# Optimization experiments

Hardware: AMD Instinct MI355X
Metric: run time of the kernel (lower is better)

Reference implementation:

```python
import jax, jax.numpy as jnp
import numpy as np

H = 1024      # embe_size / hidden size
L = 2         # layer_num
LBL = 5       # label_size
B, S = 64, 512


def setup_inputs() -> dict:
    key = jax.random.key(0)
    ks = jax.random.split(key, 7)
    sc = 1.0 / np.sqrt(H)
    inputs = jax.random.normal(ks[0], (B, S, H), dtype=jnp.float32)
    Wx = jax.random.uniform(ks[1], (L, H, 4 * H), minval=-sc, maxval=sc, dtype=jnp.float32)
    bx = jax.random.uniform(ks[2], (L, 4 * H), minval=-sc, maxval=sc, dtype=jnp.float32)
    Wh = jax.random.uniform(ks[3], (L, H, 4 * H), minval=-sc, maxval=sc, dtype=jnp.float32)
    bh = jax.random.uniform(ks[4], (L, 4 * H), minval=-sc, maxval=sc, dtype=jnp.float32)
    scp = 1.0 / np.sqrt(H)
    Wp = jax.random.uniform(ks[5], (H, LBL), minval=-scp, maxval=scp, dtype=jnp.float32)
    bp = jax.random.uniform(ks[6], (LBL,), minval=-scp, maxval=scp, dtype=jnp.float32)
    return {"inputs": inputs, "Wx": Wx, "bx": bx, "Wh": Wh, "bh": bh, "Wp": Wp, "bp": bp}


def _lstm_forward(inputs, Wx, bx, Wh, bh, Wp, bp):
    # inputs: [B,S,H] -> time-major [S,B,H]
    x = jnp.transpose(inputs, (1, 0, 2))
    n_layers = Wx.shape[0]
    bsz, hid = x.shape[1], Wx.shape[1]
    for l in range(n_layers):
        Wh_l, bh_l = Wh[l], bh[l]
        # precompute input->gate projection for all timesteps: [S,B,4H]
        xg = jnp.einsum('sbh,hg->sbg', x, Wx[l]) + bx[l]

        def step(carry, xg_t):
            h, c = carry
            feat = xg_t + h @ Wh_l + bh_l
            i, f, g, o = jnp.split(feat, 4, axis=-1)
            c = jax.nn.sigmoid(f) * c + jax.nn.sigmoid(i) * jnp.tanh(g)
            h = jnp.tanh(c) * jax.nn.sigmoid(o)
            return (h, c), h

        h0 = jnp.zeros((bsz, hid), dtype=x.dtype)
        _, x = jax.lax.scan(step, (h0, h0), xg)
        # dropout is identity at inference (eval mode)
    # max-pool over time (max_pool1d over full seq), then classify
    pooled = jnp.max(x, axis=0)  # [B,H]
    return pooled @ Wp + bp      # [B,label_size]


def reference(inputs, Wx, bx, Wh, bh, Wp, bp):
    return _lstm_forward(inputs, Wx, bx, Wh, bh, Wp, bp)
```

## Files before the change

### kernel.cpp

```cpp
#include <hip/hip_runtime.h>
#include <hip/hip_bf16.h>

typedef _Float16 half8 __attribute__((ext_vector_type(8)));
typedef _Float16 half4v __attribute__((ext_vector_type(4)));
typedef float f32x4 __attribute__((ext_vector_type(4)));
typedef unsigned int u32;
typedef unsigned long long u64;

#define BB 64
#define SS 512
#define HH 1024
#define G4 4096
#define SLOT 65536

#define SB_ARR(g) ((g) * 32)
#define SB_GLB 256
#define SB_GO(g) (288 + (g) * 32)
#define NSTEP 514

__device__ __forceinline__ float sigmf(float x) { return 1.0f / (1.0f + __expf(-x)); }
__device__ __forceinline__ float tanhfast(float x) { return 2.0f / (1.0f + __expf(-2.0f * x)) - 1.0f; }

__device__ __forceinline__ u32 aload(const u32* p) {
  return __hip_atomic_load(p, __ATOMIC_RELAXED, __HIP_MEMORY_SCOPE_AGENT);
}
__device__ __forceinline__ void wait_ge(const u32* p, u32 tgt) {
  while (aload(p) < tgt) __builtin_amdgcn_s_sleep(1);
}
__device__ __forceinline__ u32 aadd(u32* p) {
  return __hip_atomic_fetch_add(p, 1u, __ATOMIC_RELAXED, __HIP_MEMORY_SCOPE_AGENT);
}
__device__ __forceinline__ void astore(u32* p, u32 v) {
  __hip_atomic_store(p, v, __ATOMIC_RELAXED, __HIP_MEMORY_SCOPE_AGENT);
}
__device__ __forceinline__ void astore64(u64* p, u64 v) {
  __hip_atomic_store(p, v, __ATOMIC_RELAXED, __HIP_MEMORY_SCOPE_AGENT);
}

__global__ __launch_bounds__(256) void convert_x_kernel(const float* __restrict__ in,
                                                        _Float16* __restrict__ x16) {
  size_t idx = (size_t)blockIdx.x * 256 + threadIdx.x;
  int h4 = (int)(idx & 255);
  int s  = (int)((idx >> 8) & 511);
  int b  = (int)(idx >> 17);
  const float4* src = (const float4*)in;
  float4 v = src[((size_t)b * SS + s) * 256 + h4];
  half4v hv = { (_Float16)v.x, (_Float16)v.y, (_Float16)v.z, (_Float16)v.w };
  *(half4v*)(x16 + ((size_t)s * BB + b) * HH + (size_t)h4 * 4) = hv;
}

__global__ __launch_bounds__(256) void convert_w_kernel(const float* __restrict__ Wx,
                                                        const float* __restrict__ Wh,
                                                        _Float16* __restrict__ wT) {
  __shared__ float tile[32][33];
  int m = blockIdx.x >> 12;
  int t = blockIdx.x & 4095;
  int tn = t & 127, tk = t >> 7;
  int l = m & 1, which = m >> 1;
  const float* src = (which ? Wh : Wx) + (size_t)l * HH * G4;
  int tx = threadIdx.x & 31, ty = threadIdx.x >> 5;
#pragma unroll
  for (int p = 0; p < 4; ++p) {
    int k = tk * 32 + ty + 8 * p, n = tn * 32 + tx;
    tile[ty + 8 * p][tx] = src[(size_t)k * G4 + n];
  }
  __syncthreads();
  _Float16* dst = wT + (size_t)m * G4 * HH;
#pragma unroll
  for (int p = 0; p < 4; ++p) {
    int n = tn * 32 + ty + 8 * p, k = tk * 32 + tx;
    dst[(size_t)n * HH + k] = (_Float16)tile[tx][ty + 8 * p];
  }
}

__global__ __launch_bounds__(512, 2) void lstm_flow(
    const _Float16* __restrict__ x16, const _Float16* __restrict__ wT,
    const float* __restrict__ bx, const float* __restrict__ bh,
    _Float16* __restrict__ h1buf, _Float16* __restrict__ h2buf,
    float* __restrict__ hmax, u32* __restrict__ tag1, u32* __restrict__ tag2) {
  __shared__ float part[8][32][72];
  __shared__ float red[64][37];

  const int bid = blockIdx.x;
  const int layer = bid >> 7;
  const int j = bid & 127;
  const int tid = threadIdx.x;
  const int w = tid >> 6, l = tid & 63;
  const int l15 = l & 15, lg = l >> 4;
  const int rep = bid & 1;

  const _Float16* wTe = wT + (size_t)layer * G4 * HH;
  const _Float16* wTr = wT + (size_t)(2 + layer) * G4 * HH;
  const int kbase = w * 128;
  half8 Be[8], Br[8];
#pragma unroll
  for (int kk = 0; kk < 4; ++kk)
#pragma unroll
    for (int c = 0; c < 2; ++c) {
      int nl = 16 * c + l15;
      size_t gcol = (size_t)((nl & 3) * HH + 8 * j + (nl >> 2));
      Be[kk * 2 + c] = *(const half8*)(wTe + gcol * HH + kbase + 32 * kk + 8 * lg);
      Br[kk * 2 + c] = *(const half8*)(wTr + gcol * HH + kbase + 32 * kk + 8 * lg);
    }

  float bsv[32];
  float cst[8], hx[8];
#pragma unroll
  for (int cp = 0; cp < 8; ++cp) {
    cst[cp] = 0.f;
    hx[cp] = -2.f;
#pragma unroll
    for (int g = 0; g < 4; ++g)
      bsv[cp * 4 + g] = bx[layer * G4 + g * HH + 8 * j + cp] + bh[layer * G4 + g * HH + 8 * j + cp];
  }

#define POLL(TAGS, SLOTT)                                                              \
  {                                                                                    \
    const u32* tp = (TAGS) + ((size_t)(SLOTT) * 2 + rep) * 128 + 16 * w + l15;         \
    while (true) {                                                                     \
      u32 v = (l < 16) ? aload(tp) : 1u;                                               \
      if (__all(v != 0)) break;                                                        \
      __builtin_amdgcn_s_sleep(2);                                                     \
    }                                                                                  \
    asm volatile("" ::: "memory");                                                     \
  }

#pragma unroll 1
  for (int t = 0; t < SS; ++t) {
    f32x4 acc[8];
#pragma unroll
    for (int i = 0; i < 8; ++i) acc[i] = (f32x4){0.f, 0.f, 0.f, 0.f};

    {
      const _Float16* Ae;
      if (layer == 0) {
        Ae = x16 + (size_t)t * SLOT;
      } else {
        POLL(tag1, t + 1)
        Ae = h1buf + (size_t)(t + 1) * SLOT;
      }
      const _Float16* aep = Ae + (size_t)l15 * HH + kbase + 8 * lg;
      half8 a[16];
#pragma unroll
      for (int rf = 0; rf < 4; ++rf)
#pragma unroll
        for (int kk = 0; kk < 4; ++kk)
          a[rf * 4 + kk] = *(const half8*)(aep + (size_t)(16 * rf) * HH + 32 * kk);
#pragma unroll
      for (int rf = 0; rf < 4; ++rf)
#pragma unroll
        for (int kk = 0; kk < 4; ++kk) {
          acc[rf * 2 + 0] = __builtin_amdgcn_mfma_f32_16x16x32_f16(a[rf * 4 + kk], Be[kk * 2 + 0], acc[rf * 2 + 0], 0, 0, 0);
          acc[rf * 2 + 1] = __builtin_amdgcn_mfma_f32_16x16x32_f16(a[rf * 4 + kk], Be[kk * 2 + 1], acc[rf * 2 + 1], 0, 0, 0);
        }
    }

    {
      const _Float16* Ah;
      if (layer == 0) {
        if (t >= 1) POLL(tag1, t)
        Ah = h1buf + (size_t)t * SLOT;
      } else {
        if (t >= 1) POLL(tag2, t)
        Ah = h2buf + (size_t)t * SLOT;
      }
      const _Float16* ahp = Ah + (size_t)l15 * HH + kbase + 8 * lg;
      half8 a[16];
#pragma unroll
      for (int rf = 0; rf < 4; ++rf)
#pragma unroll
        for (int kk = 0; kk < 4; ++kk)
          a[rf * 4 + kk] = *(const half8*)(ahp + (size_t)(16 * rf) * HH + 32 * kk);
#pragma unroll
      for (int rf = 0; rf < 4; ++rf)
#pragma unroll
        for (int kk = 0; kk < 4; ++kk) {
          acc[rf * 2 + 0] = __builtin_amdgcn_mfma_f32_16x16x32_f16(a[rf * 4 + kk], Br[kk * 2 + 0], acc[rf * 2 + 0], 0, 0, 0);
          acc[rf * 2 + 1] = __builtin_amdgcn_mfma_f32_16x16x32_f16(a[rf * 4 + kk], Br[kk * 2 + 1], acc[rf * 2 + 1], 0, 0, 0);
        }
    }

#pragma unroll
    for (int rf = 0; rf < 4; ++rf)
#pragma unroll
      for (int c = 0; c < 2; ++c)
        *(f32x4*)&part[w][16 * c + l15][16 * rf + 4 * lg] = acc[rf * 2 + c];
    __syncthreads();

    {
      int col = tid >> 4, rq = tid & 15;
      f32x4 s = {0.f, 0.f, 0.f, 0.f};
#pragma unroll
      for (int ww = 0; ww < 8; ++ww)
        s += *(const f32x4*)&part[ww][col][4 * rq];
      red[4 * rq + 0][col] = s[0];
      red[4 * rq + 1][col] = s[1];
      red[4 * rq + 2][col] = s[2];
      red[4 * rq + 3][col] = s[3];
    }
    __syncthreads();

    if (w == 0) {
      u32 pk[4];
#pragma unroll
      for (int cp = 0; cp < 8; ++cp) {
        float vi = red[l][4 * cp + 0] + bsv[cp * 4 + 0];
        float vf = red[l][4 * cp + 1] + bsv[cp * 4 + 1];
        float vg = red[l][4 * cp + 2] + bsv[cp * 4 + 2];
        float vo = red[l][4 * cp + 3] + bsv[cp * 4 + 3];
        float ig = sigmf(vi), fg = sigmf(vf), gg = tanhfast(vg), og = sigmf(vo);
        float cn = fg * cst[cp] + ig * gg;
        cst[cp] = cn;
        float hn = tanhfast(cn) * og;
        if (layer == 1) hx[cp] = fmaxf(hx[cp], hn);
        u32 hb = (u32)__builtin_bit_cast(unsigned short, (_Float16)hn);
        if ((cp & 1) == 0) pk[cp >> 1] = hb;
        else pk[cp >> 1] |= hb << 16;
      }
      if (layer == 0 || t < SS - 1) {
        _Float16* hout = (layer == 0 ? h1buf : h2buf) + (size_t)(t + 1) * SLOT;
        u64* dst = (u64*)(hout + (size_t)l * HH + 8 * j);
        astore64(dst,     ((u64)pk[1] << 32) | pk[0]);
        astore64(dst + 1, ((u64)pk[3] << 32) | pk[2]);
        asm volatile("s_waitcnt vmcnt(0)" ::: "memory");
        if (l == 0) {
          u32* tg = (layer == 0 ? tag1 : tag2);
          astore(tg + ((size_t)(t + 1) * 2 + 0) * 128 + j, 1u);
          astore(tg + ((size_t)(t + 1) * 2 + 1) * 128 + j, 1u);
        }
      }
    }
  }
#undef POLL

  if (layer == 1 && w == 0) {
    float* hp = hmax + (size_t)l * HH + 8 * j;
    *(float4*)hp = (float4){hx[0], hx[1], hx[2], hx[3]};
    *(float4*)(hp + 4) = (float4){hx[4], hx[5], hx[6], hx[7]};
  }
}

__global__ __launch_bounds__(512, 2) void lstm_safe(
    const _Float16* __restrict__ x16, const _Float16* __restrict__ wT,
    const float* __restrict__ bx, const float* __restrict__ bh,
    _Float16* __restrict__ h1buf, _Float16* __restrict__ h2buf,
    float* __restrict__ hmax, u32* __restrict__ bar) {
  __shared__ float part[8][32][72];
  __shared__ float red[64][37];

  const int bid = blockIdx.x;
  const int layer = bid >> 7;
  const int j = bid & 127;
  const int tid = threadIdx.x;
  const int w = tid >> 6, l = tid & 63;
  const int l15 = l & 15, lg = l >> 4;
  const int grp = bid & 7;

  const _Float16* wTe = wT + (size_t)layer * G4 * HH;
  const _Float16* wTr = wT + (size_t)(2 + layer) * G4 * HH;
  const int kbase = w * 128;
  half8 Be[8], Br[8];
#pragma unroll
  for (int kk = 0; kk < 4; ++kk)
#pragma unroll
    for (int c = 0; c < 2; ++c) {
      int nl = 16 * c + l15;
      size_t gcol = (size_t)((nl & 3) * HH + 8 * j + (nl >> 2));
      Be[kk * 2 + c] = *(const half8*)(wTe + gcol * HH + kbase + 32 * kk + 8 * lg);
      Br[kk * 2 + c] = *(const half8*)(wTr + gcol * HH + kbase + 32 * kk + 8 * lg);
    }

  const int erow = tid >> 2, m2 = tid & 3;
  const int hc0 = 8 * j + 2 * m2;
  float bs[8];
  float c0 = 0.f, c1 = 0.f, hm0 = -2.f, hm1 = -2.f;
  if (tid < 256) {
#pragma unroll
    for (int dm = 0; dm < 2; ++dm)
#pragma unroll
      for (int g = 0; g < 4; ++g)
        bs[4 * dm + g] = bx[layer * G4 + g * HH + hc0 + dm] + bh[layer * G4 + g * HH + hc0 + dm];
  }

#pragma unroll 1
  for (int t = 0; t < NSTEP; ++t) {
    const bool act = (layer == 0) ? (t < SS) : (t >= 2);
    f32x4 acc[8];
#pragma unroll
    for (int i = 0; i < 8; ++i) acc[i] = (f32x4){0.f, 0.f, 0.f, 0.f};

    if (act) {
      const _Float16* Ae = (layer == 0) ? x16 + (size_t)t * SLOT
                                        : h1buf + (size_t)((t - 2) & 3) * SLOT;
      const _Float16* aep = Ae + (size_t)l15 * HH + kbase + 8 * lg;
      half8 a[16];
#pragma unroll
      for (int rf = 0; rf < 4; ++rf)
#pragma unroll
        for (int kk = 0; kk < 4; ++kk)
          a[rf * 4 + kk] = *(const half8*)(aep + (size_t)(16 * rf) * HH + 32 * kk);
#pragma unroll
      for (int rf = 0; rf < 4; ++rf)
#pragma unroll
        for (int kk = 0; kk < 4; ++kk) {
          acc[rf * 2 + 0] = __builtin_amdgcn_mfma_f32_16x16x32_f16(a[rf * 4 + kk], Be[kk * 2 + 0], acc[rf * 2 + 0], 0, 0, 0);
          acc[rf * 2 + 1] = __builtin_amdgcn_mfma_f32_16x16x32_f16(a[rf * 4 + kk], Be[kk * 2 + 1], acc[rf * 2 + 1], 0, 0, 0);
        }
    }

    if (tid == 0) {
      wait_ge(bar + SB_GO(grp), (u32)t);
      __builtin_amdgcn_fence(__ATOMIC_ACQUIRE, "agent");
    }
    __syncthreads();

    if (act) {
      const _Float16* Ah = (layer == 0) ? h1buf + (size_t)((t - 1) & 3) * SLOT
                                        : h2buf + (size_t)((t - 1) & 1) * SLOT;
      const _Float16* ahp = Ah + (size_t)l15 * HH + kbase + 8 * lg;
      half8 a[16];
#pragma unroll
      for (int rf = 0; rf < 4; ++rf)
#pragma unroll
        for (int kk = 0; kk < 4; ++kk)
          a[rf * 4 + kk] = *(const half8*)(ahp + (size_t)(16 * rf) * HH + 32 * kk);
#pragma unroll
      for (int rf = 0; rf < 4; ++rf)
#pragma unroll
        for (int kk = 0; kk < 4; ++kk) {
          acc[rf * 2 + 0] = __builtin_amdgcn_mfma_f32_16x16x32_f16(a[rf * 4 + kk], Br[kk * 2 + 0], acc[rf * 2 + 0], 0, 0, 0);
          acc[rf * 2 + 1] = __builtin_amdgcn_mfma_f32_16x16x32_f16(a[rf * 4 + kk], Br[kk * 2 + 1], acc[rf * 2 + 1], 0, 0, 0);
        }

#pragma unroll
      for (int rf = 0; rf < 4; ++rf)
#pragma unroll
        for (int c = 0; c < 2; ++c)
          *(f32x4*)&part[w][16 * c + l15][16 * rf + 4 * lg] = acc[rf * 2 + c];
      __syncthreads();

      {
        int col = tid >> 4, rq = tid & 15;
        f32x4 s = {0.f, 0.f, 0.f, 0.f};
#pragma unroll
        for (int ww = 0; ww < 8; ++ww)
          s += *(const f32x4*)&part[ww][col][4 * rq];
        red[4 * rq + 0][col] = s[0];
        red[4 * rq + 1][col] = s[1];
        red[4 * rq + 2][col] = s[2];
        red[4 * rq + 3][col] = s[3];
      }
      __syncthreads();

      if (tid < 256) {
        float v[8];
#pragma unroll
        for (int q = 0; q < 8; ++q) v[q] = red[erow][8 * m2 + q] + bs[q];
        float i0 = sigmf(v[0]), f0 = sigmf(v[1]), g0 = tanhfast(v[2]), o0 = sigmf(v[3]);
        float i1 = sigmf(v[4]), f1 = sigmf(v[5]), g1 = tanhfast(v[6]), o1 = sigmf(v[7]);
        c0 = f0 * c0 + i0 * g0;
        c1 = f1 * c1 + i1 * g1;
        float h0 = tanhfast(c0) * o0;
        float h1 = tanhfast(c1) * o1;
        if (layer == 1) { hm0 = fmaxf(hm0, h0); hm1 = fmaxf(hm1, h1); }
        _Float16* hout = (layer == 0) ? h1buf + (size_t)(t & 3) * SLOT
                                      : h2buf + (size_t)(t & 1) * SLOT;
        u32 pk = ((u32)__builtin_bit_cast(unsigned short, (_Float16)h1) << 16) |
                 (u32)__builtin_bit_cast(unsigned short, (_Float16)h0);
        astore((u32*)hout + ((erow * HH + hc0) >> 1), pk);
      }
    }

    __syncthreads();
    if (tid == 0) {
      u32 prev = aadd(bar + SB_ARR(grp));
      if (prev == 32u * (u32)(t + 1) - 1u) {
        u32 p2 = aadd(bar + SB_GLB);
        if (p2 == 8u * (u32)(t + 1) - 1u) {
#pragma unroll
          for (int gg = 0; gg < 8; ++gg)
            astore(bar + SB_GO(gg), (u32)(t + 1));
        }
      }
    }
  }

  if (layer == 1 && tid < 256) {
    hmax[erow * HH + hc0]     = hm0;
    hmax[erow * HH + hc0 + 1] = hm1;
  }
}

__global__ __launch_bounds__(320) void classify_kernel(const float* __restrict__ hmax,
                                                       const float* __restrict__ Wp,
                                                       const float* __restrict__ bp,
                                                       float* __restrict__ out) {
  int tid = threadIdx.x;
  int b = tid / 5, jj = tid % 5;
  float s = bp[jj];
  const float* hp = hmax + (size_t)b * HH;
  for (int h = 0; h < HH; ++h) s = fmaf(hp[h], Wp[h * 5 + jj], s);
  out[tid] = s;
}

extern "C" void kernel_launch(void* const* d_in, const int* in_sizes, int n_in,
                              void* d_out, int out_size, void* d_ws, size_t ws_size,
                              hipStream_t stream) {
  const float* inputs = (const float*)d_in[0];
  const float* Wx = (const float*)d_in[1];
  const float* bx = (const float*)d_in[2];
  const float* Wh = (const float*)d_in[3];
  const float* bh = (const float*)d_in[4];
  const float* Wp = (const float*)d_in[5];
  const float* bp = (const float*)d_in[6];
  float* out = (float*)d_out;

  char* ws = (char*)d_ws;
  _Float16* x16 = (_Float16*)(ws + 0);
  _Float16* wT  = (_Float16*)(ws + 67108864);

  const size_t H1_OFF = 100663296ull;
  const size_t H1_BYTES = (size_t)513 * 131072;
  const size_t H2_OFF = H1_OFF + H1_BYTES;
  const size_t H2_BYTES = (size_t)512 * 131072;
  const size_t HMAX_OFF = H2_OFF + H2_BYTES;
  const size_t TAG1_OFF = HMAX_OFF + 262144;
  const size_t TAG_BYTES = (size_t)513 * 2 * 128 * 4;
  const size_t TAG2_OFF = TAG1_OFF + TAG_BYTES;
  const size_t NEED_FAST = TAG2_OFF + TAG_BYTES;
  bool fast = ws_size >= NEED_FAST;

  convert_x_kernel<<<32768, 256, 0, stream>>>(inputs, x16);
  convert_w_kernel<<<16384, 256, 0, stream>>>(Wx, Wh, wT);

  if (fast) {
    _Float16* h1traj = (_Float16*)(ws + H1_OFF);
    _Float16* h2traj = (_Float16*)(ws + H2_OFF);
    float* hmax = (float*)(ws + HMAX_OFF);
    u32* tag1 = (u32*)(ws + TAG1_OFF);
    u32* tag2 = (u32*)(ws + TAG2_OFF);
    hipMemsetAsync(h1traj, 0, 131072, stream);
    hipMemsetAsync(h2traj, 0, 131072, stream);
    hipMemsetAsync(tag1, 0, 2 * TAG_BYTES, stream);
    lstm_flow<<<256, 512, 0, stream>>>(x16, wT, bx, bh, h1traj, h2traj, hmax, tag1, tag2);
    classify_kernel<<<1, 320, 0, stream>>>(hmax, Wp, bp, out);
  } else {
    _Float16* h1buf = (_Float16*)(ws + 100663296);
    _Float16* h2buf = (_Float16*)(ws + 101187584);
    float* hmax = (float*)(ws + 101449728);
    u32* bar = (u32*)(ws + 101711872);
    hipMemsetAsync(h1buf, 0, 524288, stream);
    hipMemsetAsync(h2buf, 0, 262144, stream);
    hipMemsetAsync(bar, 0, 8192, stream);
    lstm_safe<<<256, 512, 0, stream>>>(x16, wT, bx, bh, h1buf, h2buf, hmax, bar);
    classify_kernel<<<1, 320, 0, stream>>>(hmax, Wp, bp, out);
  }
}
```

Measured before the change: 4.306 ms.

## Software-pipeline input projection of next step ahead of recurrent wait

Moves the input-projection MFMA for step t+1 to the end of step t, after the h output is published, so that work overlaps the wait for the next recurrent tag instead of sitting on the critical path. It also changes launch bounds from 2 to 1 blocks per CU and shortens the poll sleep. The aim is to shorten the per-step serial latency of the recurrence. The risk is that layer 1 now polls tag1 for step t+2 early, which can stall when layer 0 lags, and the launch-bound change alters register allocation.

```diff
diff --git a/kernel.cpp b/kernel.cpp
--- a/kernel.cpp
+++ b/kernel.cpp
@@ -73,7 +73,7 @@
   }
 }
 
-__global__ __launch_bounds__(512, 2) void lstm_flow(
+__global__ __launch_bounds__(512, 1) void lstm_flow(
     const _Float16* __restrict__ x16, const _Float16* __restrict__ wT,
     const float* __restrict__ bx, const float* __restrict__ bh,
     _Float16* __restrict__ h1buf, _Float16* __restrict__ h2buf,
@@ -120,71 +120,54 @@
     while (true) {                                                                     \
       u32 v = (l < 16) ? aload(tp) : 1u;                                               \
       if (__all(v != 0)) break;                                                        \
-      __builtin_amdgcn_s_sleep(2);                                                     \
+      __builtin_amdgcn_s_sleep(1);                                                     \
     }                                                                                  \
     asm volatile("" ::: "memory");                                                     \
   }
 
+#define MFMA_HALF(APTR, BREG, ACC)                                                     \
+  {                                                                                    \
+    half8 a[16];                                                                       \
+    _Pragma("unroll") for (int rf = 0; rf < 4; ++rf)                                   \
+      _Pragma("unroll") for (int kk = 0; kk < 4; ++kk)                                 \
+        a[rf * 4 + kk] = *(const half8*)((APTR) + (size_t)(16 * rf) * HH + 32 * kk);   \
+    _Pragma("unroll") for (int rf = 0; rf < 4; ++rf)                                   \
+      _Pragma("unroll") for (int kk = 0; kk < 4; ++kk) {                               \
+        ACC[rf * 2 + 0] = __builtin_amdgcn_mfma_f32_16x16x32_f16(a[rf * 4 + kk], BREG[kk * 2 + 0], ACC[rf * 2 + 0], 0, 0, 0); \
+        ACC[rf * 2 + 1] = __builtin_amdgcn_mfma_f32_16x16x32_f16(a[rf * 4 + kk], BREG[kk * 2 + 1], ACC[rf * 2 + 1], 0, 0, 0); \
+      }                                                                                \
+  }
+
+  f32x4 accA[8];
+#pragma unroll
+  for (int i = 0; i < 8; ++i) accA[i] = (f32x4){0.f, 0.f, 0.f, 0.f};
+
+  if (layer == 0) {
+    const _Float16* aep = x16 + (size_t)l15 * HH + kbase + 8 * lg;
+    MFMA_HALF(aep, Be, accA)
+  } else {
+    POLL(tag1, 1)
+    const _Float16* aep = h1buf + (size_t)1 * SLOT + (size_t)l15 * HH + kbase + 8 * lg;
+    MFMA_HALF(aep, Be, accA)
+  }
+
 #pragma unroll 1
   for (int t = 0; t < SS; ++t) {
-    f32x4 acc[8];
-#pragma unroll
-    for (int i = 0; i < 8; ++i) acc[i] = (f32x4){0.f, 0.f, 0.f, 0.f};
-
+    if (t >= 1) {
+      if (layer == 0) POLL(tag1, t)
+      else            POLL(tag2, t)
+    }
     {
-      const _Float16* Ae;
-      if (layer == 0) {
-        Ae = x16 + (size_t)t * SLOT;
-      } else {
-        POLL(tag1, t + 1)
-        Ae = h1buf + (size_t)(t + 1) * SLOT;
-      }
-      const _Float16* aep = Ae + (size_t)l15 * HH + kbase + 8 * lg;
-      half8 a[16];
-#pragma unroll
-      for (int rf = 0; rf < 4; ++rf)
-#pragma unroll
-        for (int kk = 0; kk < 4; ++kk)
-          a[rf * 4 + kk] = *(const half8*)(aep + (size_t)(16 * rf) * HH + 32 * kk);
-#pragma unroll
-      for (int rf = 0; rf < 4; ++rf)
-#pragma unroll
-        for (int kk = 0; kk < 4; ++kk) {
-          acc[rf * 2 + 0] = __builtin_amdgcn_mfma_f32_16x16x32_f16(a[rf * 4 + kk], Be[kk * 2 + 0], acc[rf * 2 + 0], 0, 0, 0);
-          acc[rf * 2 + 1] = __builtin_amdgcn_mfma_f32_16x16x32_f16(a[rf * 4 + kk], Be[kk * 2 + 1], acc[rf * 2 + 1], 0, 0, 0);
-        }
-    }
-
-    {
-      const _Float16* Ah;
-      if (layer == 0) {
-        if (t >= 1) POLL(tag1, t)
-        Ah = h1buf + (size_t)t * SLOT;
-      } else {
-        if (t >= 1) POLL(tag2, t)
-        Ah = h2buf + (size_t)t * SLOT;
-      }
-      const _Float16* ahp = Ah + (size_t)l15 * HH + kbase + 8 * lg;
-      half8 a[16];
-#pragma unroll
-      for (int rf = 0; rf < 4; ++rf)
-#pragma unroll
-        for (int kk = 0; kk < 4; ++kk)
-          a[rf * 4 + kk] = *(const half8*)(ahp + (size_t)(16 * rf) * HH + 32 * kk);
-#pragma unroll
-      for (int rf = 0; rf < 4; ++rf)
-#pragma unroll
-        for (int kk = 0; kk < 4; ++kk) {
-          acc[rf * 2 + 0] = __builtin_amdgcn_mfma_f32_16x16x32_f16(a[rf * 4 + kk], Br[kk * 2 + 0], acc[rf * 2 + 0], 0, 0, 0);
-          acc[rf * 2 + 1] = __builtin_amdgcn_mfma_f32_16x16x32_f16(a[rf * 4 + kk], Br[kk * 2 + 1], acc[rf * 2 + 1], 0, 0, 0);
-        }
+      const _Float16* Ah = (layer == 0 ? h1buf : h2buf) + (size_t)t * SLOT
+                           + (size_t)l15 * HH + kbase + 8 * lg;
+      MFMA_HALF(Ah, Br, accA)
     }
 
 #pragma unroll
     for (int rf = 0; rf < 4; ++rf)
 #pragma unroll
       for (int c = 0; c < 2; ++c)
-        *(f32x4*)&part[w][16 * c + l15][16 * rf + 4 * lg] = acc[rf * 2 + c];
+        *(f32x4*)&part[w][16 * c + l15][16 * rf + 4 * lg] = accA[rf * 2 + c];
     __syncthreads();
 
     {
@@ -230,8 +213,23 @@
         }
       }
     }
+
+#pragma unroll
+    for (int i = 0; i < 8; ++i) accA[i] = (f32x4){0.f, 0.f, 0.f, 0.f};
+    const int tn = t + 1;
+    if (tn < SS) {
+      if (layer == 0) {
+        const _Float16* aep = x16 + (size_t)tn * SLOT + (size_t)l15 * HH + kbase + 8 * lg;
+        MFMA_HALF(aep, Be, accA)
+      } else {
+        POLL(tag1, tn + 1)
+        const _Float16* aep = h1buf + (size_t)(tn + 1) * SLOT + (size_t)l15 * HH + kbase + 8 * lg;
+        MFMA_HALF(aep, Be, accA)
+      }
+    }
   }
 #undef POLL
+#undef MFMA_HALF
 
   if (layer == 1 && w == 0) {
     float* hp = hmax + (size_t)l * HH + 8 * j;
```

Result: slower. 4.422 ms (+2.7%).
